# Kernel optimization log

Hardware: AMD Instinct MI355X
Metric: run time of the kernel (lower is better)

## Reference

```python
import jax, jax.numpy as jnp
import numpy as np

D = 64      # in_feats
OUT = 64    # out_feats
MEM = 4     # mem_size
NREL = 8    # num_rels
N = 20000   # num nodes
E = 50000   # num edges
FF = 16     # dim_feedforward (hardcoded in module)
NH = 4      # nhead (hardcoded)
EPS = 1e-5  # LayerNorm eps (torch default)


def _ln(x, w, b):
    m = x.mean(-1, keepdims=True)
    v = ((x - m) ** 2).mean(-1, keepdims=True)
    return (x - m) * jax.lax.rsqrt(v + EPS) * w + b


def _enc(x, Wqkv, bqkv, Wo, bo, W1, b1, W2, b2, ln1w, ln1b, ln2w, ln2b):
    # torch TransformerEncoderLayer, batch_first, post-norm, eval mode, no padding mask (all-zero mask)
    B, S, d = x.shape
    dh = d // NH
    qkv = x @ Wqkv.T + bqkv
    q, k, v = jnp.split(qkv, 3, axis=-1)
    q = q.reshape(B, S, NH, dh)
    k = k.reshape(B, S, NH, dh)
    v = v.reshape(B, S, NH, dh)
    att = jax.nn.softmax(jnp.einsum('bqhd,bkhd->bhqk', q, k) / jnp.sqrt(jnp.float32(dh)), axis=-1)
    o = jnp.einsum('bhqk,bkhd->bqhd', att, v).reshape(B, S, d) @ Wo.T + bo
    x = _ln(x + o, ln1w, ln1b)
    ff = jax.nn.relu(x @ W1.T + b1) @ W2.T + b2
    return _ln(x + ff, ln2w, ln2b)


def setup_inputs() -> dict:
    key = jax.random.key(0)
    ks = jax.random.split(key, 16)
    s = 0.05
    inp = {
        'feat': jax.random.normal(ks[0], (N, D), jnp.float32),
        'src_idx': jax.random.randint(ks[1], (E,), 0, N),
        'dst_idx': jax.random.randint(ks[2], (E,), 0, N),
        'etype': jax.random.randint(ks[3], (E,), 0, NREL),
        'Wqkv': jax.random.normal(ks[4], (3 * D, D), jnp.float32) * s,
        'bqkv': jnp.zeros((3 * D,), jnp.float32),
        'Wo': jax.random.normal(ks[5], (D, D), jnp.float32) * s,
        'bo': jnp.zeros((D,), jnp.float32),
        'W1': jax.random.normal(ks[6], (FF, D), jnp.float32) * s,
        'b1': jnp.zeros((FF,), jnp.float32),
        'W2': jax.random.normal(ks[7], (D, FF), jnp.float32) * s,
        'b2': jnp.zeros((D,), jnp.float32),
        'ln1w': jnp.ones((D,), jnp.float32),
        'ln1b': jnp.zeros((D,), jnp.float32),
        'ln2w': jnp.ones((D,), jnp.float32),
        'ln2b': jnp.zeros((D,), jnp.float32),
        'Wc': jax.random.normal(ks[8], (MEM, D), jnp.float32) * s,
        'bc': jnp.zeros((MEM,), jnp.float32),
        'CLS': jax.random.normal(ks[9], (MEM, D), jnp.float32),
        'SEP': jax.random.normal(ks[10], (D,), jnp.float32),
        'Wm': jax.random.normal(ks[11], (OUT * D, D), jnp.float32) * s,
        'h_bias': jnp.zeros((OUT,), jnp.float32),
    }
    return inp


def reference(feat, src_idx, dst_idx, etype, Wqkv, bqkv, Wo, bo, W1, b1, W2, b2,
              ln1w, ln1b, ln2w, ln2b, Wc, bc, CLS, SEP, Wm, h_bias):
    enc_args = (Wqkv, bqkv, Wo, bo, W1, b1, W2, b2, ln1w, ln1b, ln2w, ln2b)

    def cls_pass(s_, d_):
        # run the shared encoder MEM times with a different CLS token; the math
        # is identical for every relation type, so no per-etype partition needed
        B = s_.shape[0]
        outs = []
        mem = jnp.zeros((B, D), s_.dtype)
        for i in range(MEM):
            cls = jnp.broadcast_to(CLS[i], (B, D))[:, None, :]
            sep = jnp.broadcast_to(SEP, (B, D))[:, None, :]
            seq = jnp.concatenate([cls, s_[:, None, :], sep, d_[:, None, :]], axis=1)  # [B,4,D]
            t = _enc(seq, *enc_args)[:, 0, :]
            outs.append(t)
            mem = mem + t
        return mem, jnp.stack(outs)  # [B,D], [MEM,B,D]

    src = feat[src_idx]  # [E,D]
    dst = feat[dst_idx]
    mem_emb, tmps = cls_pass(src, dst)
    cat_all = tmps @ Wc.T + bc               # [MEM,E,MEM]
    w = (mem_emb @ Wm.T).reshape(E, OUT, D)  # per-edge hypernetwork weight
    msg = jnp.einsum('eoi,ei->eo', w, src)   # [E,OUT]

    # dgl fn.mean aggregation over destination nodes (0 for isolated nodes)
    cnt = jax.ops.segment_sum(jnp.ones((E,), msg.dtype), dst_idx, num_segments=N)
    agg = jax.ops.segment_sum(msg, dst_idx, num_segments=N)
    node_rep = jnp.where(cnt[:, None] > 0, agg / jnp.maximum(cnt, 1.0)[:, None], 0.0)
    node_rep = node_rep + h_bias

    # self loop (same hypernetwork path over every node)
    mem_s, _ = cls_pass(feat, feat)
    hs = (mem_s @ Wm.T).reshape(N, OUT, D)
    node_rep = node_rep + jnp.einsum('noi,ni->no', hs, feat)

    # reconstruct torch concat order of category/label: outer loop etype, inner loop mem idx
    et = etype.astype(jnp.int32)
    counts = jax.ops.segment_sum(jnp.ones((E,), jnp.int32), etype, num_segments=NREL)
    start = jnp.concatenate([jnp.zeros((1,), jnp.int32), jnp.cumsum(counts)[:-1].astype(jnp.int32)])
    order = jnp.argsort(etype, stable=True)
    rank = jnp.zeros((E,), jnp.int32).at[order].set(jnp.arange(E, dtype=jnp.int32) - start[et[order]])
    base = start[et] * MEM + rank                                            # [E]
    pos = base[None, :] + jnp.arange(MEM, dtype=jnp.int32)[:, None] * counts[et][None, :]  # [MEM,E]
    category = jnp.zeros((MEM * E, MEM), cat_all.dtype).at[pos.reshape(-1)].set(cat_all.reshape(-1, MEM))
    label = jnp.zeros((MEM * E,), jnp.int32).at[pos.reshape(-1)].set(
        jnp.repeat(jnp.arange(MEM, dtype=jnp.int32), E))
    return node_rep, label, category
```

## Files before the change

### kernel.cpp

```cpp
#include <hip/hip_runtime.h>
#include <hip/hip_bf16.h>

typedef float f32x4_t __attribute__((ext_vector_type(4)));
typedef short bf16x8_t __attribute__((ext_vector_type(8)));

#define MFMA(a, b, c) __builtin_amdgcn_mfma_f32_16x16x32_bf16(a, b, c, 0, 0, 0)

#define C_Q0   0
#define C_S00  256
#define C_S02  272
#define C_VCLS 288
#define C_VSEP 544

__device__ __forceinline__ short f2bf(float x) {
    return (short)__builtin_bit_cast(unsigned short, __float2bfloat16(x));
}
__device__ __forceinline__ float bf2f(short s) {
    return __builtin_bit_cast(float, ((unsigned)(unsigned short)s) << 16);
}
__device__ __forceinline__ float head_sum16(float v) {
#pragma unroll
    for (int off = 1; off < 16; off <<= 1) v += __shfl_xor(v, off, 64);
    return v;
}

__global__ void k_pack(const float* __restrict__ Wo, const float* __restrict__ Wqkv,
                       const float* __restrict__ W1, const float* __restrict__ W2,
                       const float* __restrict__ Wm, const float* __restrict__ Wc,
                       short* __restrict__ Bpack, short* __restrict__ WoP,
                       short* __restrict__ WkvP, short* __restrict__ W1P,
                       short* __restrict__ W2P, short* __restrict__ WcP)
{
    int tid = blockIdx.x * 256 + threadIdx.x;
    short tmp[8];
    if (tid < 32768) {
        int u = tid, lane = u & 63, nt = (u >> 6) & 3, kstep = u >> 8;
        int o = nt * 16 + (lane & 15);
        int kb = kstep * 32 + (lane >> 4) * 8;
#pragma unroll
        for (int t = 0; t < 8; t++) { int k = kb + t; tmp[t] = f2bf(Wm[(o * 64 + (k >> 6)) * 64 + (k & 63)]); }
        *(bf16x8_t*)&Bpack[(size_t)u * 8] = *(bf16x8_t*)tmp;
    } else if (tid < 33280) {
        int u = tid - 32768, lane = u & 63, nt = (u >> 6) & 3, kstep = u >> 8;
        int o = nt * 16 + (lane & 15), kb = kstep * 32 + (lane >> 4) * 8;
#pragma unroll
        for (int t = 0; t < 8; t++) tmp[t] = f2bf(Wo[o * 64 + kb + t]);
        *(bf16x8_t*)&WoP[(size_t)u * 8] = *(bf16x8_t*)tmp;
    } else if (tid < 34304) {
        int u = tid - 33280, lane = u & 63, nt = (u >> 6) & 7, kstep = u >> 9;
        int col = nt * 16 + (lane & 15), kb = kstep * 32 + (lane >> 4) * 8;
        int row = 64 + col;
#pragma unroll
        for (int t = 0; t < 8; t++) tmp[t] = f2bf(Wqkv[row * 64 + kb + t]);
        *(bf16x8_t*)&WkvP[(size_t)u * 8] = *(bf16x8_t*)tmp;
    } else if (tid < 34432) {
        int u = tid - 34304, lane = u & 63, kstep = u >> 6;
        int f = lane & 15, kb = kstep * 32 + (lane >> 4) * 8;
#pragma unroll
        for (int t = 0; t < 8; t++) tmp[t] = f2bf(W1[f * 64 + kb + t]);
        *(bf16x8_t*)&W1P[(size_t)u * 8] = *(bf16x8_t*)tmp;
    } else if (tid < 34688) {
        int u = tid - 34432, lane = u & 63, nt = u >> 6;
        int o = nt * 16 + (lane & 15), kb = (lane >> 4) * 8;
#pragma unroll
        for (int t = 0; t < 8; t++) { int k = kb + t; tmp[t] = (k < 16) ? f2bf(W2[o * 16 + k]) : (short)0; }
        *(bf16x8_t*)&W2P[(size_t)u * 8] = *(bf16x8_t*)tmp;
    } else if (tid < 34816) {
        int u = tid - 34688, lane = u & 63, kstep = u >> 6;
        int m = lane & 15, kb = kstep * 32 + (lane >> 4) * 8;
#pragma unroll
        for (int t = 0; t < 8; t++) tmp[t] = (m < 4) ? f2bf(Wc[m * 64 + kb + t]) : (short)0;
        *(bf16x8_t*)&WcP[(size_t)u * 8] = *(bf16x8_t*)tmp;
    }
}

__global__ void k_small(const float* __restrict__ Wqkv, const float* __restrict__ bqkv,
                        const float* __restrict__ CLS, const float* __restrict__ SEP,
                        float* __restrict__ consts)
{
    int lane = threadIdx.x;
    float ksep = bqkv[64 + lane], vsep = bqkv[128 + lane];
    for (int c = 0; c < 64; c++) {
        float sc = SEP[c];
        ksep += Wqkv[(64 + lane) * 64 + c] * sc;
        vsep += Wqkv[(128 + lane) * 64 + c] * sc;
    }
    consts[C_VSEP + lane] = vsep;
    for (int i = 0; i < 4; i++) {
        float q0 = bqkv[lane], kcls = bqkv[64 + lane], vcls = bqkv[128 + lane];
        for (int c = 0; c < 64; c++) {
            float cc = CLS[i * 64 + c];
            q0   += Wqkv[lane * 64 + c] * cc;
            kcls += Wqkv[(64 + lane) * 64 + c] * cc;
            vcls += Wqkv[(128 + lane) * 64 + c] * cc;
        }
        consts[C_Q0 + i * 64 + lane] = q0;
        consts[C_VCLS + i * 64 + lane] = vcls;
        float p00 = head_sum16(q0 * kcls) * 0.25f;
        float p02 = head_sum16(q0 * ksep) * 0.25f;
        if ((lane & 15) == 0) {
            consts[C_S00 + i * 4 + (lane >> 4)] = p00;
            consts[C_S02 + i * 4 + (lane >> 4)] = p02;
        }
    }
}

__global__ __launch_bounds__(256) void k_kv(const float* __restrict__ feat,
        const short* __restrict__ WkvP, const float* __restrict__ bqkv,
        float* __restrict__ knode, float* __restrict__ vnode, int N)
{
    __shared__ __align__(16) short sA[64 * 72];
    int tid = threadIdx.x, lane = tid & 63, w = tid >> 6;
    int l15 = lane & 15, lh = lane >> 4;
    int base = blockIdx.x * 64;
#pragma unroll
    for (int rr = 0; rr < 16; rr++) {
        int row = w * 16 + rr;
        int n = base + row; n = n < N ? n : N - 1;
        sA[row * 72 + lane] = f2bf(feat[(size_t)n * 64 + lane]);
    }
    __syncthreads();
    const bf16x8_t* bp = (const bf16x8_t*)WkvP;
    bf16x8_t bk0 = bp[(0 * 8 + w) * 64 + lane];
    bf16x8_t bk1 = bp[(1 * 8 + w) * 64 + lane];
    bf16x8_t bv0 = bp[(0 * 8 + 4 + w) * 64 + lane];
    bf16x8_t bv1 = bp[(1 * 8 + 4 + w) * 64 + lane];
    int kof = lh * 8;
    int col = w * 16 + l15;
    float biask = bqkv[64 + col], biasv = bqkv[128 + col];
#pragma unroll
    for (int rt = 0; rt < 4; rt++) {
        bf16x8_t a0 = *(const bf16x8_t*)&sA[(rt * 16 + l15) * 72 + kof];
        bf16x8_t a1 = *(const bf16x8_t*)&sA[(rt * 16 + l15) * 72 + 32 + kof];
        f32x4_t ak = {0.f, 0.f, 0.f, 0.f}, av = ak;
        ak = MFMA(a0, bk0, ak); ak = MFMA(a1, bk1, ak);
        av = MFMA(a0, bv0, av); av = MFMA(a1, bv1, av);
#pragma unroll
        for (int r = 0; r < 4; r++) {
            int n = base + rt * 16 + lh * 4 + r;
            if (n < N) {
                knode[(size_t)n * 64 + col] = ak[r] + biask;
                vnode[(size_t)n * 64 + col] = av[r] + biasv;
            }
        }
    }
}

struct EncW {
    const float* consts; const float* CLS; const float* bo;
    const float* b1; const float* b2;
    const float* ln1w; const float* ln1b; const float* ln2w; const float* ln2b;
    const short* WoP; const short* W1P; const short* W2P; const short* WcP;
    const float* bc;
};

__global__ __launch_bounds__(256) void k_enc(const int* __restrict__ src_idx,
        const int* __restrict__ dst_idx,
        const float* __restrict__ knode, const float* __restrict__ vnode, EncW W,
        float* __restrict__ mem_out, float* __restrict__ cat_out, int E, int M)
{
    __shared__ __align__(16) short sA[64 * 72];
    __shared__ __align__(16) short sF[64 * 40];
    int tid = threadIdx.x, lane = tid & 63, w = tid >> 6;
    int l15 = lane & 15, lh = lane >> 4;
    int base = blockIdx.x * 16;

#pragma unroll
    for (int z = 0; z < 4; z++) {
        int zz = z * 64 + lane;
        sF[(w * 16 + (zz >> 4)) * 40 + 16 + (zz & 15)] = 0;
    }

    float q0r[4], vclsr[4], s00r[4], s02r[4];
#pragma unroll
    for (int i = 0; i < 4; i++) {
        q0r[i]   = W.consts[C_Q0 + i * 64 + lane];
        vclsr[i] = W.consts[C_VCLS + i * 64 + lane];
        s00r[i]  = W.consts[C_S00 + i * 4 + lh];
        s02r[i]  = W.consts[C_S02 + i * 4 + lh];
    }
    float vsep = W.consts[C_VSEP + lane];

#pragma unroll
    for (int el = 0; el < 4; el++) {
        int eloc = w * 4 + el;
        int ge = base + eloc; int gc = ge < M ? ge : M - 1;
        int s, d;
        if (gc < E) { s = src_idx[gc]; d = dst_idx[gc]; }
        else        { s = gc - E; d = s; }
        float ks = knode[(size_t)s * 64 + lane], vs_ = vnode[(size_t)s * 64 + lane];
        float kd = knode[(size_t)d * 64 + lane], vd  = vnode[(size_t)d * 64 + lane];
#pragma unroll
        for (int i = 0; i < 4; i++) {
            float s01 = head_sum16(q0r[i] * ks) * 0.25f;
            float s03 = head_sum16(q0r[i] * kd) * 0.25f;
            float s00 = s00r[i], s02 = s02r[i];
            float mx = fmaxf(fmaxf(s00, s01), fmaxf(s02, s03));
            float e0 = __expf(s00 - mx), e1 = __expf(s01 - mx);
            float e2 = __expf(s02 - mx), e3 = __expf(s03 - mx);
            float inv = 1.0f / (e0 + e1 + e2 + e3);
            float att = (e0 * vclsr[i] + e1 * vs_ + e2 * vsep + e3 * vd) * inv;
            sA[(eloc * 4 + i) * 72 + lane] = f2bf(att);
        }
    }

    int arow = (w * 16 + l15) * 72;
    int kof = lh * 8;

    const bf16x8_t* bpo = (const bf16x8_t*)W.WoP;
    f32x4_t ac0 = {0.f,0.f,0.f,0.f}, ac1 = ac0, ac2 = ac0, ac3 = ac0;
#pragma unroll
    for (int kstep = 0; kstep < 2; kstep++) {
        bf16x8_t a = *(const bf16x8_t*)&sA[arow + kstep * 32 + kof];
        ac0 = MFMA(a, bpo[(kstep * 4 + 0) * 64 + lane], ac0);
        ac1 = MFMA(a, bpo[(kstep * 4 + 1) * 64 + lane], ac1);
        ac2 = MFMA(a, bpo[(kstep * 4 + 2) * 64 + lane], ac2);
        ac3 = MFMA(a, bpo[(kstep * 4 + 3) * 64 + lane], ac3);
    }

    float x[4][4], y[4][4];
#pragma unroll
    for (int r = 0; r < 4; r++) { x[0][r] = ac0[r]; x[1][r] = ac1[r]; x[2][r] = ac2[r]; x[3][r] = ac3[r]; }
    float lw1[4], lb1[4];
#pragma unroll
    for (int nt = 0; nt < 4; nt++) {
        float b = W.bo[nt * 16 + l15];
        lw1[nt] = W.ln1w[nt * 16 + l15]; lb1[nt] = W.ln1b[nt * 16 + l15];
#pragma unroll
        for (int r = 0; r < 4; r++) x[nt][r] += b + W.CLS[r * 64 + nt * 16 + l15];
    }
#pragma unroll
    for (int r = 0; r < 4; r++) {
        float sm = head_sum16(x[0][r] + x[1][r] + x[2][r] + x[3][r]);
        float mu = sm * 0.015625f;
        float vv = 0.f;
#pragma unroll
        for (int nt = 0; nt < 4; nt++) { float dd = x[nt][r] - mu; vv = fmaf(dd, dd, vv); }
        vv = head_sum16(vv);
        float rs = rsqrtf(vv * 0.015625f + 1e-5f);
#pragma unroll
        for (int nt = 0; nt < 4; nt++) y[nt][r] = (x[nt][r] - mu) * rs * lw1[nt] + lb1[nt];
    }
#pragma unroll
    for (int nt = 0; nt < 4; nt++)
#pragma unroll
        for (int r = 0; r < 4; r++)
            sA[(w * 16 + lh * 4 + r) * 72 + nt * 16 + l15] = f2bf(y[nt][r]);

    const bf16x8_t* bp1 = (const bf16x8_t*)W.W1P;
    f32x4_t fa = {0.f,0.f,0.f,0.f};
#pragma unroll
    for (int kstep = 0; kstep < 2; kstep++) {
        bf16x8_t a = *(const bf16x8_t*)&sA[arow + kstep * 32 + kof];
        fa = MFMA(a, bp1[kstep * 64 + lane], fa);
    }
    float b1v = W.b1[l15];
#pragma unroll
    for (int r = 0; r < 4; r++)
        sF[(w * 16 + lh * 4 + r) * 40 + l15] = f2bf(fmaxf(fa[r] + b1v, 0.f));

    const bf16x8_t* bp2 = (const bf16x8_t*)W.W2P;
    bf16x8_t af = *(const bf16x8_t*)&sF[(w * 16 + l15) * 40 + kof];
    f32x4_t z0 = {0.f,0.f,0.f,0.f}, z1 = z0, z2 = z0, z3 = z0;
    z0 = MFMA(af, bp2[0 * 64 + lane], z0);
    z1 = MFMA(af, bp2[1 * 64 + lane], z1);
    z2 = MFMA(af, bp2[2 * 64 + lane], z2);
    z3 = MFMA(af, bp2[3 * 64 + lane], z3);

    float t[4][4];
#pragma unroll
    for (int r = 0; r < 4; r++) { x[0][r] = z0[r]; x[1][r] = z1[r]; x[2][r] = z2[r]; x[3][r] = z3[r]; }
    float lw2[4], lb2[4];
#pragma unroll
    for (int nt = 0; nt < 4; nt++) {
        float b = W.b2[nt * 16 + l15];
        lw2[nt] = W.ln2w[nt * 16 + l15]; lb2[nt] = W.ln2b[nt * 16 + l15];
#pragma unroll
        for (int r = 0; r < 4; r++) x[nt][r] += b + y[nt][r];
    }
#pragma unroll
    for (int r = 0; r < 4; r++) {
        float sm = head_sum16(x[0][r] + x[1][r] + x[2][r] + x[3][r]);
        float mu = sm * 0.015625f;
        float vv = 0.f;
#pragma unroll
        for (int nt = 0; nt < 4; nt++) { float dd = x[nt][r] - mu; vv = fmaf(dd, dd, vv); }
        vv = head_sum16(vv);
        float rs = rsqrtf(vv * 0.015625f + 1e-5f);
#pragma unroll
        for (int nt = 0; nt < 4; nt++) t[nt][r] = (x[nt][r] - mu) * rs * lw2[nt] + lb2[nt];
    }

    int eloc = w * 4 + lh, ge = base + eloc;

    if (base < E) {
#pragma unroll
        for (int nt = 0; nt < 4; nt++)
#pragma unroll
            for (int r = 0; r < 4; r++)
                sA[(w * 16 + lh * 4 + r) * 72 + nt * 16 + l15] = f2bf(t[nt][r]);
        const bf16x8_t* bpc = (const bf16x8_t*)W.WcP;
        f32x4_t ca = {0.f,0.f,0.f,0.f};
#pragma unroll
        for (int kstep = 0; kstep < 2; kstep++) {
            bf16x8_t a = *(const bf16x8_t*)&sA[arow + kstep * 32 + kof];
            ca = MFMA(a, bpc[kstep * 64 + lane], ca);
        }
        if (l15 < 4 && ge < E) {
            float bcv = W.bc[l15];
#pragma unroll
            for (int r = 0; r < 4; r++)
                cat_out[((size_t)r * E + ge) * 4 + l15] = ca[r] + bcv;
        }
    }

    if (ge < M) {
#pragma unroll
        for (int nt = 0; nt < 4; nt++)
            mem_out[(size_t)ge * 64 + nt * 16 + l15] = t[nt][0] + t[nt][1] + t[nt][2] + t[nt][3];
    }
}

__global__ __launch_bounds__(256, 3) void k_hyper(
        const float* __restrict__ feat, const int* __restrict__ src_idx,
        const int* __restrict__ dst_idx, const float* __restrict__ memall,
        const short* __restrict__ Bpack,
        float* __restrict__ agg, float* __restrict__ selfm, int E, int M)
{
    __shared__ short xsT[64 * 132];
    __shared__ __align__(16) short sB[2][8192];
    int tid = threadIdx.x, lane = tid & 63, w = tid >> 6;
    int l15 = lane & 15, lh = lane >> 4, koff = lh * 8;
    int base = blockIdx.x * 128;

    const bf16x8_t* bp = (const bf16x8_t*)Bpack;

    auto stage = [&](int c, int buf) {
#pragma unroll
        for (int jj = 0; jj < 4; ++jj) {
            int j = w * 4 + jj;
            int il_ic = j >> 3, q = j & 7;
            const short* src = (const short*)(bp + (size_t)(c * 2 + il_ic) * 512
                                              + (q >> 2) * 256 + (q & 3) * 64 + lane);
            short* dst = &sB[buf][j * 512];
            __builtin_amdgcn_global_load_lds(
                (const __attribute__((address_space(1))) void*)src,
                (__attribute__((address_space(3))) void*)dst, 16, 0, 0);
        }
    };

    stage(0, 0);

    for (int rr = 0; rr < 32; ++rr) {
        int row = w * 32 + rr, gr = base + row;
        float xv = 0.f;
        if (gr < M) {
            int xi = gr < E ? src_idx[gr] : gr - E;
            xv = feat[(size_t)xi * 64 + lane];
        }
        xsT[lane * 132 + row] = f2bf(xv);
    }

    bf16x8_t am[2][2];
#pragma unroll
    for (int tt = 0; tt < 2; ++tt) {
        int gr = base + w * 32 + tt * 16 + l15;
        const float* mp = memall + (size_t)(gr < M ? gr : 0) * 64 + koff;
#pragma unroll
        for (int kk = 0; kk < 2; ++kk)
#pragma unroll
            for (int t = 0; t < 8; ++t)
                am[tt][kk][t] = f2bf(mp[kk * 32 + t]);
    }

    f32x4_t out[2][4];
#pragma unroll
    for (int tt = 0; tt < 2; ++tt)
#pragma unroll
        for (int nt = 0; nt < 4; ++nt) out[tt][nt] = (f32x4_t){0.f, 0.f, 0.f, 0.f};
    const f32x4_t ZERO = {0.f, 0.f, 0.f, 0.f};

    int xrow0 = w * 32 + lh * 4;

    int cur = 0;
    for (int c = 0; c < 32; ++c) {
        if (c + 1 < 32) {
            stage(c + 1, cur ^ 1);
            asm volatile("s_waitcnt vmcnt(4)" ::: "memory");
        } else {
            asm volatile("s_waitcnt vmcnt(0)" ::: "memory");
        }
        __builtin_amdgcn_s_barrier();
#pragma unroll
        for (int ic = 0; ic < 2; ++ic) {
            int i = c * 2 + ic;
            unsigned long long xw0 = *(const unsigned long long*)&xsT[i * 132 + xrow0];
            unsigned long long xw1 = *(const unsigned long long*)&xsT[i * 132 + xrow0 + 16];
            float x0[4], x1[4];
            {
                unsigned lo0 = (unsigned)xw0, hi0 = (unsigned)(xw0 >> 32);
                unsigned lo1 = (unsigned)xw1, hi1 = (unsigned)(xw1 >> 32);
                x0[0] = __builtin_bit_cast(float, lo0 << 16);
                x0[1] = __builtin_bit_cast(float, lo0 & 0xffff0000u);
                x0[2] = __builtin_bit_cast(float, hi0 << 16);
                x0[3] = __builtin_bit_cast(float, hi0 & 0xffff0000u);
                x1[0] = __builtin_bit_cast(float, lo1 << 16);
                x1[1] = __builtin_bit_cast(float, lo1 & 0xffff0000u);
                x1[2] = __builtin_bit_cast(float, hi1 << 16);
                x1[3] = __builtin_bit_cast(float, hi1 & 0xffff0000u);
            }
            const bf16x8_t* bfr = (const bf16x8_t*)&sB[cur][ic * 4096];
            f32x4_t P0[4], P1[4];
            __builtin_amdgcn_s_setprio(1);
#pragma unroll
            for (int nt = 0; nt < 4; ++nt) {
                bf16x8_t B0 = bfr[nt * 64 + lane];
                bf16x8_t B1 = bfr[(4 + nt) * 64 + lane];
                P0[nt] = MFMA(am[0][0], B0, ZERO);
                P1[nt] = MFMA(am[1][0], B0, ZERO);
                P0[nt] = MFMA(am[0][1], B1, P0[nt]);
                P1[nt] = MFMA(am[1][1], B1, P1[nt]);
            }
            __builtin_amdgcn_s_setprio(0);
#pragma unroll
            for (int nt = 0; nt < 4; ++nt)
#pragma unroll
                for (int r = 0; r < 4; ++r) {
                    out[0][nt][r] = fmaf(x0[r], P0[nt][r], out[0][nt][r]);
                    out[1][nt][r] = fmaf(x1[r], P1[nt][r], out[1][nt][r]);
                }
        }
        __builtin_amdgcn_s_barrier();
        cur ^= 1;
    }

#pragma unroll
    for (int tt = 0; tt < 2; ++tt) {
        int orow = w * 32 + tt * 16 + lh * 4;
        int di[4];
#pragma unroll
        for (int r = 0; r < 4; ++r) {
            int grow = base + orow + r;
            di[r] = (grow < E) ? dst_idx[grow] : 0;
        }
#pragma unroll
        for (int nt = 0; nt < 4; ++nt) {
            int o = nt * 16 + l15;
#pragma unroll
            for (int r = 0; r < 4; ++r) {
                int grow = base + orow + r;
                if (grow < M) {
                    float v = out[tt][nt][r];
                    if (grow < E) atomicAdd(&agg[(size_t)di[r] * 64 + o], v);
                    else selfm[(size_t)(grow - E) * 64 + o] = v;
                }
            }
        }
    }
}

__global__ void k_fin(const float* __restrict__ agg, const int* __restrict__ cnt,
                      const float* __restrict__ selfm, const float* __restrict__ h_bias,
                      float* __restrict__ outp, int N)
{
    int t = blockIdx.x * 256 + threadIdx.x;
    if (t < N * 64) {
        int n = t >> 6, o = t & 63;
        int c = cnt[n];
        float av = (c > 0) ? agg[t] / (float)c : 0.f;
        outp[t] = av + h_bias[o] + selfm[t];
    }
}

__global__ void k_hist(const int* __restrict__ etype, const int* __restrict__ dst,
                       int* __restrict__ hist, int* __restrict__ cnt, int E)
{
    __shared__ int h[8];
    int tid = threadIdx.x;
    if (tid < 8) h[tid] = 0;
    __syncthreads();
    int e = blockIdx.x * 256 + tid;
    if (e < E) {
        atomicAdd(&h[etype[e]], 1);
        atomicAdd(&cnt[dst[e]], 1);
    }
    __syncthreads();
    if (tid < 8) hist[blockIdx.x * 8 + tid] = h[tid];
}

__global__ void k_scan(const int* __restrict__ hist, int* __restrict__ chunkoff,
                       int* __restrict__ startg, int* __restrict__ countsg, int nch)
{
    int lane = threadIdx.x;
    int g = lane & 7, seg = lane >> 3;
    int per = (nch + 7) / 8;
    int c0 = seg * per, c1 = c0 + per; if (c1 > nch) c1 = nch;
    int sum = 0;
    for (int c = c0; c < c1; c++) sum += hist[c * 8 + g];
    int pre = 0, tot = 0;
#pragma unroll
    for (int s2 = 0; s2 < 8; s2++) {
        int v = __shfl(sum, s2 * 8 + g, 64);
        tot += v;
        if (s2 < seg) pre += v;
    }
    int run = pre;
    for (int c = c0; c < c1; c++) { chunkoff[c * 8 + g] = run; run += hist[c * 8 + g]; }
    if (seg == 0) {
        countsg[g] = tot;
        int sg = 0;
#pragma unroll
        for (int g2 = 0; g2 < 8; g2++) { int v = __shfl(tot, g2, 64); if (g2 < g) sg += v; }
        startg[g] = sg;
    }
}

__global__ __launch_bounds__(256) void k_scatter(const int* __restrict__ etype,
        const float* __restrict__ cat_all,
        const int* __restrict__ chunkoff, const int* __restrict__ startg,
        const int* __restrict__ countsg,
        float* __restrict__ out_label, float* __restrict__ out_cat, int E)
{
    __shared__ int wc[4][8];
    int tid = threadIdx.x, lane = tid & 63, w = tid >> 6;
    int chunk = blockIdx.x;
    int e = chunk * 256 + w * 64 + lane;
    int et = (e < E) ? etype[e] : -1;
    unsigned long long mk[8];
#pragma unroll
    for (int g = 0; g < 8; g++) mk[g] = __ballot(et == g);
    if (lane < 8) wc[w][lane] = (int)__popcll(mk[lane]);
    __syncthreads();
    if (et >= 0) {
        unsigned long long lt = (1ull << lane) - 1ull;
        int myr = chunkoff[chunk * 8 + et] + (int)__popcll(mk[et] & lt);
#pragma unroll
        for (int w2 = 0; w2 < 4; w2++) if (w2 < w) myr += wc[w2][et];
        int sg = startg[et], cg = countsg[et];
        size_t pbase = (size_t)sg * 4 + myr;
#pragma unroll
        for (int i = 0; i < 4; i++) {
            size_t pos = pbase + (size_t)i * cg;
            out_label[pos] = (float)i;
            const float* ca = &cat_all[((size_t)i * E + e) * 4];
            float4 cv = {ca[0], ca[1], ca[2], ca[3]};
            *(float4*)&out_cat[pos * 4] = cv;
        }
    }
}

extern "C" void kernel_launch(void* const* d_in, const int* in_sizes, int n_in,
                              void* d_out, int out_size, void* d_ws, size_t ws_size,
                              hipStream_t stream)
{
    const float* feat    = (const float*)d_in[0];
    const int*   src_idx = (const int*)d_in[1];
    const int*   dst_idx = (const int*)d_in[2];
    const int*   etype   = (const int*)d_in[3];
    const float* Wqkv    = (const float*)d_in[4];
    const float* bqkv    = (const float*)d_in[5];
    const float* Wo      = (const float*)d_in[6];
    const float* bo      = (const float*)d_in[7];
    const float* W1      = (const float*)d_in[8];
    const float* b1      = (const float*)d_in[9];
    const float* W2      = (const float*)d_in[10];
    const float* b2      = (const float*)d_in[11];
    const float* ln1w    = (const float*)d_in[12];
    const float* ln1b    = (const float*)d_in[13];
    const float* ln2w    = (const float*)d_in[14];
    const float* ln2b    = (const float*)d_in[15];
    const float* Wc      = (const float*)d_in[16];
    const float* bc      = (const float*)d_in[17];
    const float* CLS     = (const float*)d_in[18];
    const float* SEP     = (const float*)d_in[19];
    const float* Wm      = (const float*)d_in[20];
    const float* h_bias  = (const float*)d_in[21];

    const int N = in_sizes[0] / 64;
    const int E = in_sizes[1];
    const int M = E + N;
    const int NCH = (E + 255) / 256;

    float* ws = (float*)d_ws;
    size_t off = 0;
    auto alloc = [&](size_t n) { float* p = ws + off; off += (n + 63) & ~(size_t)63; return p; };
    float* knode   = alloc((size_t)N * 64);
    float* vnode   = alloc((size_t)N * 64);
    float* mem_all = alloc((size_t)M * 64);
    float* cat_all = alloc((size_t)E * 16);
    float* agg     = alloc((size_t)N * 64 + N);
    int*   cnt     = (int*)(agg + (size_t)N * 64);
    float* selfm   = alloc((size_t)N * 64);
    float* consts  = alloc(1024);
    short* Bpack   = (short*)alloc(131072);
    short* WoP     = (short*)alloc(2048);
    short* WkvP    = (short*)alloc(4096);
    short* W1P     = (short*)alloc(512);
    short* W2P     = (short*)alloc(1024);
    short* WcP     = (short*)alloc(512);
    int*   hist    = (int*)alloc(NCH * 8);
    int*   chunkoff= (int*)alloc(NCH * 8);
    int*   startg  = (int*)alloc(8);
    int*   countsg = (int*)alloc(8);

    float* out_node  = (float*)d_out;
    float* out_label = out_node + (size_t)N * 64;
    float* out_cat   = out_label + (size_t)4 * E;

    hipMemsetAsync(agg, 0, ((size_t)N * 64 + N) * sizeof(float), stream);

    k_pack<<<136, 256, 0, stream>>>(Wo, Wqkv, W1, W2, Wm, Wc, Bpack, WoP, WkvP, W1P, W2P, WcP);
    k_small<<<1, 64, 0, stream>>>(Wqkv, bqkv, CLS, SEP, consts);
    k_hist<<<NCH, 256, 0, stream>>>(etype, dst_idx, hist, cnt, E);
    k_scan<<<1, 64, 0, stream>>>(hist, chunkoff, startg, countsg, NCH);

    k_kv<<<(N + 63) / 64, 256, 0, stream>>>(feat, WkvP, bqkv, knode, vnode, N);

    EncW W{consts, CLS, bo, b1, b2, ln1w, ln1b, ln2w, ln2b, WoP, W1P, W2P, WcP, bc};

    k_enc<<<(M + 15) / 16, 256, 0, stream>>>(src_idx, dst_idx, knode, vnode, W,
                                             mem_all, cat_all, E, M);

    k_hyper<<<(M + 127) / 128, 256, 0, stream>>>(feat, src_idx, dst_idx, mem_all, Bpack,
                                                 agg, selfm, E, M);

    k_fin<<<(N * 64 + 255) / 256, 256, 0, stream>>>(agg, cnt, selfm, h_bias, out_node, N);

    k_scatter<<<NCH, 256, 0, stream>>>(etype, cat_all, chunkoff, startg, countsg,
                                       out_label, out_cat, E);
}
```

Measured before the change: 165.3 us.

## Fold CLS query into key projection and merge small prep kernels

The CLS query is folded algebraically into the key weights, producing a 16-wide per-node score table (4 mem slots × 4 heads) in place of a 64-wide key tensor. The encoder then reads precomputed scores, which cuts gather traffic and removes per-edge head reductions. Separately, the pack, constant and histogram kernels are merged into a single launch, and the fused-weight computation is placed in the scan kernel. The cost is extra bf16 rounding of the fused weights and a serial one-wave kernel doing more work.

New measurement: 150.9 us. 1.1x faster.

```diff
diff --git a/kernel.cpp b/kernel.cpp
--- a/kernel.cpp
+++ b/kernel.cpp
@@ -24,90 +24,161 @@
     return v;
 }
 
-__global__ void k_pack(const float* __restrict__ Wo, const float* __restrict__ Wqkv,
+__global__ void k_prep(const float* __restrict__ Wo, const float* __restrict__ Wqkv,
                        const float* __restrict__ W1, const float* __restrict__ W2,
                        const float* __restrict__ Wm, const float* __restrict__ Wc,
+                       const float* __restrict__ bqkv,
+                       const float* __restrict__ CLS, const float* __restrict__ SEP,
+                       const int* __restrict__ etype, const int* __restrict__ dst,
                        short* __restrict__ Bpack, short* __restrict__ WoP,
                        short* __restrict__ WkvP, short* __restrict__ W1P,
-                       short* __restrict__ W2P, short* __restrict__ WcP)
-{
-    int tid = blockIdx.x * 256 + threadIdx.x;
+                       short* __restrict__ W2P, short* __restrict__ WcP,
+                       float* __restrict__ consts,
+                       int* __restrict__ hist, int* __restrict__ cnt, int E)
+{
+    int bx = blockIdx.x;
+    if (bx < 136) {
+        int tid = bx * 256 + threadIdx.x;
+        short tmp[8];
+        if (tid < 32768) {
+            int u = tid, lane = u & 63, nt = (u >> 6) & 3, kstep = u >> 8;
+            int o = nt * 16 + (lane & 15);
+            int kb = kstep * 32 + (lane >> 4) * 8;
+#pragma unroll
+            for (int t = 0; t < 8; t++) { int k = kb + t; tmp[t] = f2bf(Wm[(o * 64 + (k >> 6)) * 64 + (k & 63)]); }
+            *(bf16x8_t*)&Bpack[(size_t)u * 8] = *(bf16x8_t*)tmp;
+        } else if (tid < 33280) {
+            int u = tid - 32768, lane = u & 63, nt = (u >> 6) & 3, kstep = u >> 8;
+            int o = nt * 16 + (lane & 15), kb = kstep * 32 + (lane >> 4) * 8;
+#pragma unroll
+            for (int t = 0; t < 8; t++) tmp[t] = f2bf(Wo[o * 64 + kb + t]);
+            *(bf16x8_t*)&WoP[(size_t)u * 8] = *(bf16x8_t*)tmp;
+        } else if (tid < 34304) {
+            int u = tid - 33280, lane = u & 63, nt = (u >> 6) & 7, kstep = u >> 9;
+            int col = nt * 16 + (lane & 15), kb = kstep * 32 + (lane >> 4) * 8;
+            int row = 64 + col;
+#pragma unroll
+            for (int t = 0; t < 8; t++) tmp[t] = f2bf(Wqkv[row * 64 + kb + t]);
+            *(bf16x8_t*)&WkvP[(size_t)u * 8] = *(bf16x8_t*)tmp;
+        } else if (tid < 34432) {
+            int u = tid - 34304, lane = u & 63, kstep = u >> 6;
+            int f = lane & 15, kb = kstep * 32 + (lane >> 4) * 8;
+#pragma unroll
+            for (int t = 0; t < 8; t++) tmp[t] = f2bf(W1[f * 64 + kb + t]);
+            *(bf16x8_t*)&W1P[(size_t)u * 8] = *(bf16x8_t*)tmp;
+        } else if (tid < 34688) {
+            int u = tid - 34432, lane = u & 63, nt = u >> 6;
+            int o = nt * 16 + (lane & 15), kb = (lane >> 4) * 8;
+#pragma unroll
+            for (int t = 0; t < 8; t++) { int k = kb + t; tmp[t] = (k < 16) ? f2bf(W2[o * 16 + k]) : (short)0; }
+            *(bf16x8_t*)&W2P[(size_t)u * 8] = *(bf16x8_t*)tmp;
+        } else if (tid < 34816) {
+            int u = tid - 34688, lane = u & 63, kstep = u >> 6;
+            int m = lane & 15, kb = kstep * 32 + (lane >> 4) * 8;
+#pragma unroll
+            for (int t = 0; t < 8; t++) tmp[t] = (m < 4) ? f2bf(Wc[m * 64 + kb + t]) : (short)0;
+            *(bf16x8_t*)&WcP[(size_t)u * 8] = *(bf16x8_t*)tmp;
+        }
+    } else if (bx == 136) {
+        if (threadIdx.x < 64) {
+            int lane = threadIdx.x;
+            float ksep = bqkv[64 + lane], vsep = bqkv[128 + lane];
+            for (int c = 0; c < 64; c++) {
+                float sc = SEP[c];
+                ksep += Wqkv[(64 + lane) * 64 + c] * sc;
+                vsep += Wqkv[(128 + lane) * 64 + c] * sc;
+            }
+            consts[C_VSEP + lane] = vsep;
+            for (int i = 0; i < 4; i++) {
+                float q0 = bqkv[lane], kcls = bqkv[64 + lane], vcls = bqkv[128 + lane];
+                for (int c = 0; c < 64; c++) {
+                    float cc = CLS[i * 64 + c];
+                    q0   += Wqkv[lane * 64 + c] * cc;
+                    kcls += Wqkv[(64 + lane) * 64 + c] * cc;
+                    vcls += Wqkv[(128 + lane) * 64 + c] * cc;
+                }
+                consts[C_Q0 + i * 64 + lane] = q0;
+                consts[C_VCLS + i * 64 + lane] = vcls;
+                float p00 = head_sum16(q0 * kcls) * 0.25f;
+                float p02 = head_sum16(q0 * ksep) * 0.25f;
+                if ((lane & 15) == 0) {
+                    consts[C_S00 + i * 4 + (lane >> 4)] = p00;
+                    consts[C_S02 + i * 4 + (lane >> 4)] = p02;
+                }
+            }
+        }
+    } else {
+        __shared__ int h[8];
+        int chunk = bx - 137;
+        int tid = threadIdx.x;
+        if (tid < 8) h[tid] = 0;
+        __syncthreads();
+        int e = chunk * 256 + tid;
+        if (e < E) {
+            atomicAdd(&h[etype[e]], 1);
+            atomicAdd(&cnt[dst[e]], 1);
+        }
+        __syncthreads();
+        if (tid < 8) hist[chunk * 8 + tid] = h[tid];
+    }
+}
+
+__global__ void k_scan(const int* __restrict__ hist, int* __restrict__ chunkoff,
+                       int* __restrict__ startg, int* __restrict__ countsg, int nch,
+                       const float* __restrict__ consts, const float* __restrict__ Wqkv,
+                       const float* __restrict__ bqkv,
+                       short* __restrict__ WqkP, float* __restrict__ bqk)
+{
+    int lane = threadIdx.x;
+    int g = lane & 7, seg = lane >> 3;
+    int per = (nch + 7) / 8;
+    int c0 = seg * per, c1 = c0 + per; if (c1 > nch) c1 = nch;
+    int sum = 0;
+    for (int c = c0; c < c1; c++) sum += hist[c * 8 + g];
+    int pre = 0, tot = 0;
+#pragma unroll
+    for (int s2 = 0; s2 < 8; s2++) {
+        int v = __shfl(sum, s2 * 8 + g, 64);
+        tot += v;
+        if (s2 < seg) pre += v;
+    }
+    int run = pre;
+    for (int c = c0; c < c1; c++) { chunkoff[c * 8 + g] = run; run += hist[c * 8 + g]; }
+    if (seg == 0) {
+        countsg[g] = tot;
+        int sg = 0;
+#pragma unroll
+        for (int g2 = 0; g2 < 8; g2++) { int v = __shfl(tot, g2, 64); if (g2 < g) sg += v; }
+        startg[g] = sg;
+    }
+
+    int ih = lane & 15, ii = ih & 3, hh = ih >> 2;
+    int lh8 = (lane >> 4) * 8;
     short tmp[8];
-    if (tid < 32768) {
-        int u = tid, lane = u & 63, nt = (u >> 6) & 3, kstep = u >> 8;
-        int o = nt * 16 + (lane & 15);
-        int kb = kstep * 32 + (lane >> 4) * 8;
-#pragma unroll
-        for (int t = 0; t < 8; t++) { int k = kb + t; tmp[t] = f2bf(Wm[(o * 64 + (k >> 6)) * 64 + (k & 63)]); }
-        *(bf16x8_t*)&Bpack[(size_t)u * 8] = *(bf16x8_t*)tmp;
-    } else if (tid < 33280) {
-        int u = tid - 32768, lane = u & 63, nt = (u >> 6) & 3, kstep = u >> 8;
-        int o = nt * 16 + (lane & 15), kb = kstep * 32 + (lane >> 4) * 8;
-#pragma unroll
-        for (int t = 0; t < 8; t++) tmp[t] = f2bf(Wo[o * 64 + kb + t]);
-        *(bf16x8_t*)&WoP[(size_t)u * 8] = *(bf16x8_t*)tmp;
-    } else if (tid < 34304) {
-        int u = tid - 33280, lane = u & 63, nt = (u >> 6) & 7, kstep = u >> 9;
-        int col = nt * 16 + (lane & 15), kb = kstep * 32 + (lane >> 4) * 8;
-        int row = 64 + col;
-#pragma unroll
-        for (int t = 0; t < 8; t++) tmp[t] = f2bf(Wqkv[row * 64 + kb + t]);
-        *(bf16x8_t*)&WkvP[(size_t)u * 8] = *(bf16x8_t*)tmp;
-    } else if (tid < 34432) {
-        int u = tid - 34304, lane = u & 63, kstep = u >> 6;
-        int f = lane & 15, kb = kstep * 32 + (lane >> 4) * 8;
-#pragma unroll
-        for (int t = 0; t < 8; t++) tmp[t] = f2bf(W1[f * 64 + kb + t]);
-        *(bf16x8_t*)&W1P[(size_t)u * 8] = *(bf16x8_t*)tmp;
-    } else if (tid < 34688) {
-        int u = tid - 34432, lane = u & 63, nt = u >> 6;
-        int o = nt * 16 + (lane & 15), kb = (lane >> 4) * 8;
-#pragma unroll
-        for (int t = 0; t < 8; t++) { int k = kb + t; tmp[t] = (k < 16) ? f2bf(W2[o * 16 + k]) : (short)0; }
-        *(bf16x8_t*)&W2P[(size_t)u * 8] = *(bf16x8_t*)tmp;
-    } else if (tid < 34816) {
-        int u = tid - 34688, lane = u & 63, kstep = u >> 6;
-        int m = lane & 15, kb = kstep * 32 + (lane >> 4) * 8;
-#pragma unroll
-        for (int t = 0; t < 8; t++) tmp[t] = (m < 4) ? f2bf(Wc[m * 64 + kb + t]) : (short)0;
-        *(bf16x8_t*)&WcP[(size_t)u * 8] = *(bf16x8_t*)tmp;
-    }
-}
-
-__global__ void k_small(const float* __restrict__ Wqkv, const float* __restrict__ bqkv,
-                        const float* __restrict__ CLS, const float* __restrict__ SEP,
-                        float* __restrict__ consts)
-{
-    int lane = threadIdx.x;
-    float ksep = bqkv[64 + lane], vsep = bqkv[128 + lane];
-    for (int c = 0; c < 64; c++) {
-        float sc = SEP[c];
-        ksep += Wqkv[(64 + lane) * 64 + c] * sc;
-        vsep += Wqkv[(128 + lane) * 64 + c] * sc;
-    }
-    consts[C_VSEP + lane] = vsep;
-    for (int i = 0; i < 4; i++) {
-        float q0 = bqkv[lane], kcls = bqkv[64 + lane], vcls = bqkv[128 + lane];
-        for (int c = 0; c < 64; c++) {
-            float cc = CLS[i * 64 + c];
-            q0   += Wqkv[lane * 64 + c] * cc;
-            kcls += Wqkv[(64 + lane) * 64 + c] * cc;
-            vcls += Wqkv[(128 + lane) * 64 + c] * cc;
-        }
-        consts[C_Q0 + i * 64 + lane] = q0;
-        consts[C_VCLS + i * 64 + lane] = vcls;
-        float p00 = head_sum16(q0 * kcls) * 0.25f;
-        float p02 = head_sum16(q0 * ksep) * 0.25f;
-        if ((lane & 15) == 0) {
-            consts[C_S00 + i * 4 + (lane >> 4)] = p00;
-            consts[C_S02 + i * 4 + (lane >> 4)] = p02;
-        }
+#pragma unroll
+    for (int kstep = 0; kstep < 2; kstep++) {
+#pragma unroll
+        for (int t = 0; t < 8; t++) {
+            int k = kstep * 32 + lh8 + t;
+            float s = 0.f;
+            for (int u = 0; u < 16; u++)
+                s += consts[C_Q0 + ii * 64 + hh * 16 + u] * Wqkv[(64 + hh * 16 + u) * 64 + k];
+            tmp[t] = f2bf(0.25f * s);
+        }
+        *(bf16x8_t*)&WqkP[(size_t)(kstep * 64 + lane) * 8] = *(bf16x8_t*)tmp;
+    }
+    if (lane < 16) {
+        float s = 0.f;
+        for (int u = 0; u < 16; u++)
+            s += consts[C_Q0 + ii * 64 + hh * 16 + u] * bqkv[64 + hh * 16 + u];
+        bqk[lane] = 0.25f * s;
     }
 }
 
 __global__ __launch_bounds__(256) void k_kv(const float* __restrict__ feat,
-        const short* __restrict__ WkvP, const float* __restrict__ bqkv,
-        float* __restrict__ knode, float* __restrict__ vnode, int N)
+        const short* __restrict__ WkvP, const short* __restrict__ WqkP,
+        const float* __restrict__ bqkv, const float* __restrict__ bqk,
+        float* __restrict__ vnode, float* __restrict__ qs, int N)
 {
     __shared__ __align__(16) short sA[64 * 72];
     int tid = threadIdx.x, lane = tid & 63, w = tid >> 6;
@@ -121,26 +192,32 @@
     }
     __syncthreads();
     const bf16x8_t* bp = (const bf16x8_t*)WkvP;
-    bf16x8_t bk0 = bp[(0 * 8 + w) * 64 + lane];
-    bf16x8_t bk1 = bp[(1 * 8 + w) * 64 + lane];
     bf16x8_t bv0 = bp[(0 * 8 + 4 + w) * 64 + lane];
     bf16x8_t bv1 = bp[(1 * 8 + 4 + w) * 64 + lane];
+    bf16x8_t bq0 = ((const bf16x8_t*)WqkP)[lane];
+    bf16x8_t bq1 = ((const bf16x8_t*)WqkP)[64 + lane];
     int kof = lh * 8;
     int col = w * 16 + l15;
-    float biask = bqkv[64 + col], biasv = bqkv[128 + col];
+    float biasv = bqkv[128 + col];
+    float bqv = bqk[l15];
 #pragma unroll
     for (int rt = 0; rt < 4; rt++) {
         bf16x8_t a0 = *(const bf16x8_t*)&sA[(rt * 16 + l15) * 72 + kof];
         bf16x8_t a1 = *(const bf16x8_t*)&sA[(rt * 16 + l15) * 72 + 32 + kof];
-        f32x4_t ak = {0.f, 0.f, 0.f, 0.f}, av = ak;
-        ak = MFMA(a0, bk0, ak); ak = MFMA(a1, bk1, ak);
+        f32x4_t av = {0.f, 0.f, 0.f, 0.f};
         av = MFMA(a0, bv0, av); av = MFMA(a1, bv1, av);
 #pragma unroll
         for (int r = 0; r < 4; r++) {
             int n = base + rt * 16 + lh * 4 + r;
-            if (n < N) {
-                knode[(size_t)n * 64 + col] = ak[r] + biask;
-                vnode[(size_t)n * 64 + col] = av[r] + biasv;
+            if (n < N) vnode[(size_t)n * 64 + col] = av[r] + biasv;
+        }
+        if (w == 0) {
+            f32x4_t aq = {0.f, 0.f, 0.f, 0.f};
+            aq = MFMA(a0, bq0, aq); aq = MFMA(a1, bq1, aq);
+#pragma unroll
+            for (int r = 0; r < 4; r++) {
+                int n = base + rt * 16 + lh * 4 + r;
+                if (n < N) qs[(size_t)n * 16 + l15] = aq[r] + bqv;
             }
         }
     }
@@ -156,7 +233,7 @@
 
 __global__ __launch_bounds__(256) void k_enc(const int* __restrict__ src_idx,
         const int* __restrict__ dst_idx,
-        const float* __restrict__ knode, const float* __restrict__ vnode, EncW W,
+        const float* __restrict__ vnode, const float* __restrict__ qs, EncW W,
         float* __restrict__ mem_out, float* __restrict__ cat_out, int E, int M)
 {
     __shared__ __align__(16) short sA[64 * 72];
@@ -171,10 +248,9 @@
         sF[(w * 16 + (zz >> 4)) * 40 + 16 + (zz & 15)] = 0;
     }
 
-    float q0r[4], vclsr[4], s00r[4], s02r[4];
+    float vclsr[4], s00r[4], s02r[4];
 #pragma unroll
     for (int i = 0; i < 4; i++) {
-        q0r[i]   = W.consts[C_Q0 + i * 64 + lane];
         vclsr[i] = W.consts[C_VCLS + i * 64 + lane];
         s00r[i]  = W.consts[C_S00 + i * 4 + lh];
         s02r[i]  = W.consts[C_S02 + i * 4 + lh];
@@ -188,12 +264,15 @@
         int s, d;
         if (gc < E) { s = src_idx[gc]; d = dst_idx[gc]; }
         else        { s = gc - E; d = s; }
-        float ks = knode[(size_t)s * 64 + lane], vs_ = vnode[(size_t)s * 64 + lane];
-        float kd = knode[(size_t)d * 64 + lane], vd  = vnode[(size_t)d * 64 + lane];
+        float vs_ = vnode[(size_t)s * 64 + lane];
+        float vd  = vnode[(size_t)d * 64 + lane];
+        float4 qh_s = *(const float4*)&qs[(size_t)s * 16 + lh * 4];
+        float4 qh_d = *(const float4*)&qs[(size_t)d * 16 + lh * 4];
+        float qsv[4] = {qh_s.x, qh_s.y, qh_s.z, qh_s.w};
+        float qdv[4] = {qh_d.x, qh_d.y, qh_d.z, qh_d.w};
 #pragma unroll
         for (int i = 0; i < 4; i++) {
-            float s01 = head_sum16(q0r[i] * ks) * 0.25f;
-            float s03 = head_sum16(q0r[i] * kd) * 0.25f;
+            float s01 = qsv[i], s03 = qdv[i];
             float s00 = s00r[i], s02 = s02r[i];
             float mx = fmaxf(fmaxf(s00, s01), fmaxf(s02, s03));
             float e0 = __expf(s00 - mx), e1 = __expf(s01 - mx);
@@ -469,49 +548,6 @@
         int c = cnt[n];
         float av = (c > 0) ? agg[t] / (float)c : 0.f;
         outp[t] = av + h_bias[o] + selfm[t];
-    }
-}
-
-__global__ void k_hist(const int* __restrict__ etype, const int* __restrict__ dst,
-                       int* __restrict__ hist, int* __restrict__ cnt, int E)
-{
-    __shared__ int h[8];
-    int tid = threadIdx.x;
-    if (tid < 8) h[tid] = 0;
-    __syncthreads();
-    int e = blockIdx.x * 256 + tid;
-    if (e < E) {
-        atomicAdd(&h[etype[e]], 1);
-        atomicAdd(&cnt[dst[e]], 1);
-    }
-    __syncthreads();
-    if (tid < 8) hist[blockIdx.x * 8 + tid] = h[tid];
-}
-
-__global__ void k_scan(const int* __restrict__ hist, int* __restrict__ chunkoff,
-                       int* __restrict__ startg, int* __restrict__ countsg, int nch)
-{
-    int lane = threadIdx.x;
-    int g = lane & 7, seg = lane >> 3;
-    int per = (nch + 7) / 8;
-    int c0 = seg * per, c1 = c0 + per; if (c1 > nch) c1 = nch;
-    int sum = 0;
-    for (int c = c0; c < c1; c++) sum += hist[c * 8 + g];
-    int pre = 0, tot = 0;
-#pragma unroll
-    for (int s2 = 0; s2 < 8; s2++) {
-        int v = __shfl(sum, s2 * 8 + g, 64);
-        tot += v;
-        if (s2 < seg) pre += v;
-    }
-    int run = pre;
-    for (int c = c0; c < c1; c++) { chunkoff[c * 8 + g] = run; run += hist[c * 8 + g]; }
-    if (seg == 0) {
-        countsg[g] = tot;
-        int sg = 0;
-#pragma unroll
-        for (int g2 = 0; g2 < 8; g2++) { int v = __shfl(tot, g2, 64); if (g2 < g) sg += v; }
-        startg[g] = sg;
     }
 }
 
@@ -584,7 +620,7 @@
     float* ws = (float*)d_ws;
     size_t off = 0;
     auto alloc = [&](size_t n) { float* p = ws + off; off += (n + 63) & ~(size_t)63; return p; };
-    float* knode   = alloc((size_t)N * 64);
+    float* qs      = alloc((size_t)N * 16);
     float* vnode   = alloc((size_t)N * 64);
     float* mem_all = alloc((size_t)M * 64);
     float* cat_all = alloc((size_t)E * 16);
@@ -598,6 +634,8 @@
     short* W1P     = (short*)alloc(512);
     short* W2P     = (short*)alloc(1024);
     short* WcP     = (short*)alloc(512);
+    short* WqkP    = (short*)alloc(512);
+    float* bqk     = alloc(64);
     int*   hist    = (int*)alloc(NCH * 8);
     int*   chunkoff= (int*)alloc(NCH * 8);
     int*   startg  = (int*)alloc(8);
@@ -609,16 +647,17 @@
 
     hipMemsetAsync(agg, 0, ((size_t)N * 64 + N) * sizeof(float), stream);
 
-    k_pack<<<136, 256, 0, stream>>>(Wo, Wqkv, W1, W2, Wm, Wc, Bpack, WoP, WkvP, W1P, W2P, WcP);
-    k_small<<<1, 64, 0, stream>>>(Wqkv, bqkv, CLS, SEP, consts);
-    k_hist<<<NCH, 256, 0, stream>>>(etype, dst_idx, hist, cnt, E);
-    k_scan<<<1, 64, 0, stream>>>(hist, chunkoff, startg, countsg, NCH);
-
-    k_kv<<<(N + 63) / 64, 256, 0, stream>>>(feat, WkvP, bqkv, knode, vnode, N);
+    k_prep<<<137 + NCH, 256, 0, stream>>>(Wo, Wqkv, W1, W2, Wm, Wc, bqkv, CLS, SEP,
+                                          etype, dst_idx, Bpack, WoP, WkvP, W1P, W2P, WcP,
+                                          consts, hist, cnt, E);
+    k_scan<<<1, 64, 0, stream>>>(hist, chunkoff, startg, countsg, NCH,
+                                 consts, Wqkv, bqkv, WqkP, bqk);
+
+    k_kv<<<(N + 63) / 64, 256, 0, stream>>>(feat, WkvP, WqkP, bqkv, bqk, vnode, qs, N);
 
     EncW W{consts, CLS, bo, b1, b2, ln1w, ln1b, ln2w, ln2b, WoP, W1P, W2P, WcP, bc};
 
-    k_enc<<<(M + 15) / 16, 256, 0, stream>>>(src_idx, dst_idx, knode, vnode, W,
+    k_enc<<<(M + 15) / 16, 256, 0, stream>>>(src_idx, dst_idx, vnode, qs, W,
                                              mem_all, cat_all, E, M);
 
     k_hyper<<<(M + 127) / 128, 256, 0, stream>>>(feat, src_idx, dst_idx, mem_all, Bpack,
```
